# Kernel tuning notes

Hardware: AMD Instinct MI355X
Metric: run time of the kernel (lower is better)

The kernel has to match this reference:

```python
import jax, jax.numpy as jnp
import numpy as np

B, N, MW, H, C, K = 64, 8192, 128, 8, 1024, 3
HD = C // H  # head width = 128


def setup_inputs() -> dict:
    key = jax.random.key(0)
    ks = jax.random.split(key, 16)
    s = 0.02
    return {
        "control_state": jax.random.normal(ks[0], (B, C), jnp.float32),
        "memory": jax.random.normal(ks[1], (B, N, MW), jnp.float32),
        "prev_weights": jax.nn.softmax(jax.random.normal(ks[2], (B, H, N), jnp.float32), axis=-1),
        "defaults": jax.nn.softmax(jax.random.normal(ks[3], (B, H, N), jnp.float32), axis=-1),
        "W_head": s * jax.random.normal(ks[4], (C, H * HD), jnp.float32),
        "b_head": jnp.zeros((H, HD), jnp.float32),
        "W_reset": s * jax.random.normal(ks[5], (H, HD, 1), jnp.float32),
        "b_reset": jnp.zeros((H, 1), jnp.float32),
        "W_key": s * jax.random.normal(ks[6], (H, HD, MW), jnp.float32),
        "b_key": jnp.zeros((H, MW), jnp.float32),
        "W_beta": s * jax.random.normal(ks[7], (H, HD, 1), jnp.float32),
        "b_beta": jnp.zeros((H, 1), jnp.float32),
        "W_gate": s * jax.random.normal(ks[8], (H, HD, 1), jnp.float32),
        "b_gate": jnp.zeros((H, 1), jnp.float32),
        "W_shift": s * jax.random.normal(ks[9], (H, HD, K), jnp.float32),
        "b_shift": jnp.zeros((H, K), jnp.float32),
        "W_gamma": s * jax.random.normal(ks[10], (H, HD, 1), jnp.float32),
        "b_gamma": jnp.zeros((H, 1), jnp.float32),
        "merge_w": jax.random.normal(ks[11], (H,), jnp.float32) * 0.3 + 1.0 / H,
    }


def reference(control_state, memory, prev_weights, defaults, W_head, b_head,
              W_reset, b_reset, W_key, b_key, W_beta, b_beta, W_gate, b_gate,
              W_shift, b_shift, W_gamma, b_gamma, merge_w):
    eps = 1e-8
    # head projection: [B,C] -> [B,H,HD]
    heads = (control_state @ W_head).reshape(-1, H, HD) + b_head
    # sigmoid reset gate: convex blend of prior weights with defaults
    reset_p = jax.nn.sigmoid(jnp.einsum('bhd,hdo->bho', heads, W_reset) + b_reset)  # [B,H,1]
    weights = prev_weights * (1.0 - reset_p) + defaults * reset_p
    # NTM addressing parameters (per-head linear maps)
    key_ = jnp.einsum('bhd,hdw->bhw', heads, W_key) + b_key          # [B,H,MW]
    beta = jax.nn.softplus(jnp.einsum('bhd,hdo->bho', heads, W_beta) + b_beta)   # [B,H,1]
    gate = jax.nn.sigmoid(jnp.einsum('bhd,hdo->bho', heads, W_gate) + b_gate)    # [B,H,1]
    shift = jax.nn.softmax(jnp.einsum('bhd,hdk->bhk', heads, W_shift) + b_shift, axis=-1)  # [B,H,K]
    gamma = 1.0 + jax.nn.softplus(jnp.einsum('bhd,hdo->bho', heads, W_gamma) + b_gamma)    # [B,H,1]
    # content addressing: sharpened cosine similarity softmax over memory slots
    sim = jnp.einsum('bhw,bnw->bhn', key_, memory)
    sim = sim / (jnp.linalg.norm(key_, axis=-1, keepdims=True)
                 * jnp.linalg.norm(memory, axis=-1)[:, None, :] + eps)
    content = jax.nn.softmax(beta * sim, axis=-1)                    # [B,H,N]
    # interpolate with (possibly reset) prior weights
    w_g = gate * content + (1.0 - gate) * weights
    # location addressing: circular convolution with shift kernel symmetric around 0
    w_s = sum(shift[..., j:j + 1] * jnp.roll(w_g, j - K // 2, axis=-1) for j in range(K))
    # sharpening
    w_pow = (w_s + eps) ** gamma
    new_w = w_pow / jnp.sum(w_pow, axis=-1, keepdims=True)           # [B,H,N]
    # read: per-head attention matmul against memory, then weighted head merge
    headed = jnp.einsum('bhn,bnw->bhw', new_w, memory)               # [B,H,MW]
    out = jnp.einsum('bhw,h->bw', headed, merge_w)                   # [B,MW]
    return out, new_w
```

## Files before the change

### kernel.cpp

```cpp
#include <hip/hip_runtime.h>
#include <hip/hip_bf16.h>
#include <math.h>

#define Bb 64
#define Nn 8192
#define MWw 128
#define Hh 8
#define Cc 1024
#define HDd 128
#define Kk 3

__device__ __forceinline__ float dot4(float4 a, float4 b) {
  return a.x*b.x + a.y*b.y + a.z*b.z + a.w*b.w;
}
__device__ __forceinline__ float sigmoidf_(float x) { return 1.0f / (1.0f + __expf(-x)); }
__device__ __forceinline__ float softplusf_(float x) {
  return fmaxf(x, 0.0f) + log1pf(__expf(-fabsf(x)));
}

__global__ __launch_bounds__(1024) void k_params(
    const float* __restrict__ cs, const float* __restrict__ W_head, const float* __restrict__ b_head,
    const float* __restrict__ W_reset, const float* __restrict__ b_reset,
    const float* __restrict__ W_key, const float* __restrict__ b_key,
    const float* __restrict__ W_beta, const float* __restrict__ b_beta,
    const float* __restrict__ W_gate, const float* __restrict__ b_gate,
    const float* __restrict__ W_shift, const float* __restrict__ b_shift,
    const float* __restrict__ W_gamma, const float* __restrict__ b_gamma,
    float* __restrict__ key_ws, float* __restrict__ params)
{
  int bh = blockIdx.x;
  int b = bh >> 3, h = bh & 7;
  int t = threadIdx.x;
  int d = t & 127, sl = t >> 7;
  __shared__ float red[8][128];
  __shared__ float head_s[128];
  __shared__ float key_s[128];

  const float* csb = cs + b * Cc + sl * 128;
  const float* w0 = W_head + (size_t)(sl * 128) * (Hh * HDd) + h * HDd + d;
  float acc = 0.0f;
  #pragma unroll 8
  for (int c = 0; c < 128; ++c) acc = fmaf(csb[c], w0[(size_t)c * (Hh * HDd)], acc);
  red[sl][d] = acc;
  __syncthreads();
  if (t < 128) {
    float s = b_head[h * HDd + t];
    #pragma unroll
    for (int j = 0; j < 8; ++j) s += red[j][t];
    head_s[t] = s;
  }
  __syncthreads();

  {
    const float* wk = W_key + (size_t)h * HDd * MWw + (sl * 16) * MWw + d;
    float ka = 0.0f;
    #pragma unroll
    for (int dd = 0; dd < 16; ++dd) ka = fmaf(head_s[sl * 16 + dd], wk[dd * MWw], ka);
    red[sl][d] = ka;
  }
  __syncthreads();
  if (t < 128) {
    float kv = b_key[h * MWw + t];
    #pragma unroll
    for (int j = 0; j < 8; ++j) kv += red[j][t];
    key_ws[bh * MWw + t] = kv;
    key_s[t] = kv;
  }
  __syncthreads();

  float hd = head_s[d];
  float v;
  switch (sl) {
    case 0: v = hd * W_reset[h * HDd + d]; break;
    case 1: v = hd * W_beta[h * HDd + d]; break;
    case 2: v = hd * W_gate[h * HDd + d]; break;
    case 3: v = hd * W_gamma[h * HDd + d]; break;
    case 4: v = hd * W_shift[(h * HDd + d) * Kk + 0]; break;
    case 5: v = hd * W_shift[(h * HDd + d) * Kk + 1]; break;
    case 6: v = hd * W_shift[(h * HDd + d) * Kk + 2]; break;
    default: v = key_s[d] * key_s[d]; break;
  }
  red[sl][d] = v;
  __syncthreads();
  for (int s = 64; s > 0; s >>= 1) {
    if (d < s) red[sl][d] += red[sl][d + s];
    __syncthreads();
  }
  if (t == 0) {
    float reset = sigmoidf_(red[0][0] + b_reset[h]);
    float beta  = softplusf_(red[1][0] + b_beta[h]);
    float gate  = sigmoidf_(red[2][0] + b_gate[h]);
    float gamma = 1.0f + softplusf_(red[3][0] + b_gamma[h]);
    float a0 = red[4][0] + b_shift[h * Kk + 0];
    float a1 = red[5][0] + b_shift[h * Kk + 1];
    float a2 = red[6][0] + b_shift[h * Kk + 2];
    float mx = fmaxf(a0, fmaxf(a1, a2));
    float e0 = __expf(a0 - mx), e1 = __expf(a1 - mx), e2 = __expf(a2 - mx);
    float inv = 1.0f / (e0 + e1 + e2);
    float* P = params + bh * 8;
    P[0] = reset; P[1] = beta; P[2] = gate; P[3] = gamma;
    P[4] = e0 * inv; P[5] = e1 * inv; P[6] = e2 * inv;
    P[7] = sqrtf(red[7][0]);
  }
}

__global__ __launch_bounds__(256, 2) void k_sim(
    const float* __restrict__ mem, const float* __restrict__ key_ws,
    const float* __restrict__ params, float* __restrict__ e_ws, float* __restrict__ Z)
{
  int b = blockIdx.y, chunk = blockIdx.x;
  int t = threadIdx.x;
  int lane = t & 63, wid = t >> 6;
  int sub = lane & 7, rid = lane >> 3;
  __shared__ float4 keys[8][32];
  __shared__ float betas[8], knorms[8];
  if (t < 8) { betas[t] = params[(b * 8 + t) * 8 + 1]; knorms[t] = params[(b * 8 + t) * 8 + 7]; }
  {
    int h = t >> 5, q = t & 31;
    keys[h][q] = ((const float4*)key_ws)[(b * 8 + h) * 32 + q];
  }
  __syncthreads();

  float4 kreg[8][4];
  #pragma unroll
  for (int h2 = 0; h2 < 8; ++h2) {
    kreg[h2][0] = keys[h2][sub];
    kreg[h2][1] = keys[h2][sub + 8];
    kreg[h2][2] = keys[h2][sub + 16];
    kreg[h2][3] = keys[h2][sub + 24];
  }

  const float4* m4 = (const float4*)mem + (size_t)b * Nn * 32;
  float beta = betas[sub], kn = knorms[sub];
  float zloc = 0.0f;
  int n0 = chunk * 512;

  #pragma unroll 1
  for (int itr = 0; itr < 8; ++itr) {
    int nb = n0 + itr * 64 + wid * 16 + rid;
    float4 m[2][4];
    float nrm[2];
    float acc[2][8];
    #pragma unroll
    for (int r = 0; r < 2; ++r) {
      const float4* rp = m4 + (size_t)(nb + r * 8) * 32 + sub;
      m[r][0] = rp[0]; m[r][1] = rp[8]; m[r][2] = rp[16]; m[r][3] = rp[24];
    }
    #pragma unroll
    for (int r = 0; r < 2; ++r) {
      nrm[r] = dot4(m[r][0], m[r][0]) + dot4(m[r][1], m[r][1])
             + dot4(m[r][2], m[r][2]) + dot4(m[r][3], m[r][3]);
      #pragma unroll
      for (int h2 = 0; h2 < 8; ++h2) {
        acc[r][h2] = dot4(m[r][0], kreg[h2][0]) + dot4(m[r][1], kreg[h2][1])
                   + dot4(m[r][2], kreg[h2][2]) + dot4(m[r][3], kreg[h2][3]);
      }
    }
    #pragma unroll
    for (int r = 0; r < 2; ++r) {
      float* a = acc[r];
      bool h1 = (sub & 1) != 0;
      float v40 = (h1 ? a[1] : a[0]) + __shfl_xor(h1 ? a[0] : a[1], 1, 64);
      float v41 = (h1 ? a[3] : a[2]) + __shfl_xor(h1 ? a[2] : a[3], 1, 64);
      float v42 = (h1 ? a[5] : a[4]) + __shfl_xor(h1 ? a[4] : a[5], 1, 64);
      float v43 = (h1 ? a[7] : a[6]) + __shfl_xor(h1 ? a[6] : a[7], 1, 64);
      bool h2b = (sub & 2) != 0;
      float v20 = (h2b ? v41 : v40) + __shfl_xor(h2b ? v40 : v41, 2, 64);
      float v21 = (h2b ? v43 : v42) + __shfl_xor(h2b ? v42 : v43, 2, 64);
      bool h4 = (sub & 4) != 0;
      float dsum = (h4 ? v21 : v20) + __shfl_xor(h4 ? v20 : v21, 4, 64);
      float nr = nrm[r];
      nr += __shfl_xor(nr, 1, 64);
      nr += __shfl_xor(nr, 2, 64);
      nr += __shfl_xor(nr, 4, 64);
      float s = beta * dsum / (kn * sqrtf(nr) + 1e-8f);
      float e = __expf(s - beta);
      e_ws[(size_t)(b * 8 + sub) * Nn + (nb + r * 8)] = e;
      zloc += e;
    }
  }
  zloc += __shfl_xor(zloc, 8, 64);
  zloc += __shfl_xor(zloc, 16, 64);
  zloc += __shfl_xor(zloc, 32, 64);
  if (lane < 8) atomicAdd(&Z[b * 8 + lane], zloc);
}

__global__ __launch_bounds__(256) void k_conv(
    const float* __restrict__ e_ws, const float* __restrict__ prev, const float* __restrict__ defw,
    const float* __restrict__ params, const float* __restrict__ Z,
    float* __restrict__ wp, float* __restrict__ S)
{
  int chunk = blockIdx.x, h = blockIdx.y, b = blockIdx.z;
  int bh = b * 8 + h, t = threadIdx.x;
  __shared__ float wg[2050];
  const float* P = params + bh * 8;
  float reset = P[0], gate = P[2], gamma = P[3], s0 = P[4], s1 = P[5], s2 = P[6];
  float invZg = gate / Z[bh];
  float om = 1.0f - gate, omr = 1.0f - reset;
  size_t base = (size_t)bh * Nn;
  int n0 = chunk * 2048;

  for (int it = 0; it < 8; ++it) {
    int l = it * 256 + t;
    int n = n0 + l;
    float e = e_ws[base + n], pv = prev[base + n], dv = defw[base + n];
    wg[1 + l] = invZg * e + om * (pv * omr + dv * reset);
  }
  if (t < 2) {
    int n = (t == 0) ? ((n0 + Nn - 1) & (Nn - 1)) : ((n0 + 2048) & (Nn - 1));
    float e = e_ws[base + n], pv = prev[base + n], dv = defw[base + n];
    wg[(t == 0) ? 0 : 2049] = invZg * e + om * (pv * omr + dv * reset);
  }
  __syncthreads();

  float sacc = 0.0f;
  for (int it = 0; it < 8; ++it) {
    int l = it * 256 + t;
    float wsv = s0 * wg[l + 2] + s1 * wg[l + 1] + s2 * wg[l];
    float wpv = __expf(gamma * __logf(wsv + 1e-8f));
    wp[base + n0 + l] = wpv;
    sacc += wpv;
  }
  sacc += __shfl_xor(sacc, 1, 64);
  sacc += __shfl_xor(sacc, 2, 64);
  sacc += __shfl_xor(sacc, 4, 64);
  sacc += __shfl_xor(sacc, 8, 64);
  sacc += __shfl_xor(sacc, 16, 64);
  sacc += __shfl_xor(sacc, 32, 64);
  __shared__ float sred[4];
  if ((t & 63) == 0) sred[t >> 6] = sacc;
  __syncthreads();
  if (t == 0) atomicAdd(&S[bh], sred[0] + sred[1] + sred[2] + sred[3]);
}

__global__ __launch_bounds__(256) void k_norm(
    float* __restrict__ wp, const float* __restrict__ S, const float* __restrict__ merge_w,
    float* __restrict__ coef)
{
  int b = blockIdx.y; int n0 = blockIdx.x * 1024; int t = threadIdx.x;
  __shared__ float invS[8], mw[8];
  if (t < 8) { invS[t] = 1.0f / S[b * 8 + t]; mw[t] = merge_w[t]; }
  __syncthreads();
  for (int it = 0; it < 4; ++it) {
    int n = n0 + it * 256 + t;
    float cf = 0.0f;
    #pragma unroll
    for (int h = 0; h < 8; ++h) {
      size_t idx = (size_t)(b * 8 + h) * Nn + n;
      float v = wp[idx] * invS[h];
      wp[idx] = v;
      cf = fmaf(mw[h], v, cf);
    }
    coef[(size_t)b * Nn + n] = cf;
  }
}

__global__ __launch_bounds__(256) void k_read(
    const float* __restrict__ mem, const float* __restrict__ coef, float* __restrict__ out)
{
  int b = blockIdx.y; int n0 = blockIdx.x * 512; int t = threadIdx.x;
  int w4 = t & 31, rg = t >> 5;
  const float4* m4 = (const float4*)mem + (size_t)b * Nn * 32;
  const float* cf = coef + (size_t)b * Nn;
  float4 acc = make_float4(0.0f, 0.0f, 0.0f, 0.0f);
  #pragma unroll 4
  for (int it = 0; it < 64; ++it) {
    int n = n0 + it * 8 + rg;
    float c = cf[n];
    float4 m = m4[(size_t)n * 32 + w4];
    acc.x = fmaf(c, m.x, acc.x);
    acc.y = fmaf(c, m.y, acc.y);
    acc.z = fmaf(c, m.z, acc.z);
    acc.w = fmaf(c, m.w, acc.w);
  }
  __shared__ float4 red4[256];
  red4[t] = acc;
  __syncthreads();
  if (t < 32) {
    float4 s = red4[t];
    #pragma unroll
    for (int j = 1; j < 8; ++j) {
      float4 o = red4[t + 32 * j];
      s.x += o.x; s.y += o.y; s.z += o.z; s.w += o.w;
    }
    atomicAdd(&out[b * MWw + t * 4 + 0], s.x);
    atomicAdd(&out[b * MWw + t * 4 + 1], s.y);
    atomicAdd(&out[b * MWw + t * 4 + 2], s.z);
    atomicAdd(&out[b * MWw + t * 4 + 3], s.w);
  }
}

extern "C" void kernel_launch(void* const* d_in, const int* in_sizes, int n_in,
                              void* d_out, int out_size, void* d_ws, size_t ws_size,
                              hipStream_t stream)
{
  const float* cs      = (const float*)d_in[0];
  const float* mem     = (const float*)d_in[1];
  const float* prev    = (const float*)d_in[2];
  const float* defw    = (const float*)d_in[3];
  const float* W_head  = (const float*)d_in[4];
  const float* b_head  = (const float*)d_in[5];
  const float* W_reset = (const float*)d_in[6];
  const float* b_reset = (const float*)d_in[7];
  const float* W_key   = (const float*)d_in[8];
  const float* b_key   = (const float*)d_in[9];
  const float* W_beta  = (const float*)d_in[10];
  const float* b_beta  = (const float*)d_in[11];
  const float* W_gate  = (const float*)d_in[12];
  const float* b_gate  = (const float*)d_in[13];
  const float* W_shift = (const float*)d_in[14];
  const float* b_shift = (const float*)d_in[15];
  const float* W_gamma = (const float*)d_in[16];
  const float* b_gamma = (const float*)d_in[17];
  const float* merge_w = (const float*)d_in[18];

  float* out  = (float*)d_out;
  float* neww = out + Bb * MWw;

  float* ws_f   = (float*)d_ws;
  float* key_ws = ws_f;
  float* params = ws_f + 65536;
  float* Zacc   = ws_f + 69632;
  float* Sacc   = ws_f + 70144;
  float* e_ws   = ws_f + 70656;
  float* coef   = ws_f + 70656 + 4194304;

  hipMemsetAsync(Zacc, 0, 1024 * sizeof(float), stream);
  hipMemsetAsync(out, 0, Bb * MWw * sizeof(float), stream);

  k_params<<<dim3(Bb * Hh), dim3(1024), 0, stream>>>(
      cs, W_head, b_head, W_reset, b_reset, W_key, b_key, W_beta, b_beta,
      W_gate, b_gate, W_shift, b_shift, W_gamma, b_gamma, key_ws, params);
  k_sim<<<dim3(16, Bb), dim3(256), 0, stream>>>(mem, key_ws, params, e_ws, Zacc);
  k_conv<<<dim3(4, Hh, Bb), dim3(256), 0, stream>>>(e_ws, prev, defw, params, Zacc, neww, Sacc);
  k_norm<<<dim3(8, Bb), dim3(256), 0, stream>>>(neww, Sacc, merge_w, coef);
  k_read<<<dim3(16, Bb), dim3(256), 0, stream>>>(mem, coef, out);
}
```

Before: 505.6 us.

## Fuse normalization into read kernel, stage sim outputs in LDS, vectorize conv

Merges the weight-normalization kernel into the memory-read kernel, so the per-slot coefficient lives in shared memory instead of a global workspace buffer and one launch is dropped. The similarity kernel now buffers its exp values in shared memory and writes them out as coalesced float4 rows instead of strided scalar stores. The convolution/sharpen kernel is rewritten to use float4 loads and stores, with the halo elements kept at the end of the shared buffer. In exchange, the similarity kernel uses more shared memory, which may lower occupancy.

```diff
diff --git a/kernel.cpp b/kernel.cpp
--- a/kernel.cpp
+++ b/kernel.cpp
@@ -114,6 +114,7 @@
   int sub = lane & 7, rid = lane >> 3;
   __shared__ float4 keys[8][32];
   __shared__ float betas[8], knorms[8];
+  __shared__ float e_s[8][520];
   if (t < 8) { betas[t] = params[(b * 8 + t) * 8 + 1]; knorms[t] = params[(b * 8 + t) * 8 + 7]; }
   {
     int h = t >> 5, q = t & 31;
@@ -175,7 +176,7 @@
       nr += __shfl_xor(nr, 4, 64);
       float s = beta * dsum / (kn * sqrtf(nr) + 1e-8f);
       float e = __expf(s - beta);
-      e_ws[(size_t)(b * 8 + sub) * Nn + (nb + r * 8)] = e;
+      e_s[sub][(nb + r * 8) - n0] = e;
       zloc += e;
     }
   }
@@ -183,6 +184,15 @@
   zloc += __shfl_xor(zloc, 16, 64);
   zloc += __shfl_xor(zloc, 32, 64);
   if (lane < 8) atomicAdd(&Z[b * 8 + lane], zloc);
+  __syncthreads();
+
+  #pragma unroll
+  for (int j = 0; j < 4; ++j) {
+    int idx = j * 256 + t;
+    int h = idx >> 7, q = idx & 127;
+    float4 v = *(const float4*)&e_s[h][q * 4];
+    ((float4*)(e_ws + (size_t)(b * 8 + h) * Nn + n0))[q] = v;
+  }
 }
 
 __global__ __launch_bounds__(256) void k_conv(
@@ -192,7 +202,7 @@
 {
   int chunk = blockIdx.x, h = blockIdx.y, b = blockIdx.z;
   int bh = b * 8 + h, t = threadIdx.x;
-  __shared__ float wg[2050];
+  __shared__ float wg[2052];
   const float* P = params + bh * 8;
   float reset = P[0], gate = P[2], gamma = P[3], s0 = P[4], s1 = P[5], s2 = P[6];
   float invZg = gate / Z[bh];
@@ -200,26 +210,48 @@
   size_t base = (size_t)bh * Nn;
   int n0 = chunk * 2048;
 
-  for (int it = 0; it < 8; ++it) {
-    int l = it * 256 + t;
-    int n = n0 + l;
-    float e = e_ws[base + n], pv = prev[base + n], dv = defw[base + n];
-    wg[1 + l] = invZg * e + om * (pv * omr + dv * reset);
+  const float4* e4p = (const float4*)(e_ws + base + n0);
+  const float4* p4p = (const float4*)(prev + base + n0);
+  const float4* d4p = (const float4*)(defw + base + n0);
+  #pragma unroll
+  for (int it = 0; it < 2; ++it) {
+    int idx4 = it * 256 + t;
+    float4 e = e4p[idx4], pv = p4p[idx4], dv = d4p[idx4];
+    float4 w;
+    w.x = invZg * e.x + om * (pv.x * omr + dv.x * reset);
+    w.y = invZg * e.y + om * (pv.y * omr + dv.y * reset);
+    w.z = invZg * e.z + om * (pv.z * omr + dv.z * reset);
+    w.w = invZg * e.w + om * (pv.w * omr + dv.w * reset);
+    *(float4*)&wg[idx4 * 4] = w;
   }
   if (t < 2) {
     int n = (t == 0) ? ((n0 + Nn - 1) & (Nn - 1)) : ((n0 + 2048) & (Nn - 1));
     float e = e_ws[base + n], pv = prev[base + n], dv = defw[base + n];
-    wg[(t == 0) ? 0 : 2049] = invZg * e + om * (pv * omr + dv * reset);
+    wg[2048 + t] = invZg * e + om * (pv * omr + dv * reset);
   }
   __syncthreads();
 
   float sacc = 0.0f;
-  for (int it = 0; it < 8; ++it) {
-    int l = it * 256 + t;
-    float wsv = s0 * wg[l + 2] + s1 * wg[l + 1] + s2 * wg[l];
-    float wpv = __expf(gamma * __logf(wsv + 1e-8f));
-    wp[base + n0 + l] = wpv;
-    sacc += wpv;
+  float4* wp4 = (float4*)(wp + base + n0);
+  #pragma unroll
+  for (int it = 0; it < 2; ++it) {
+    int idx4 = it * 256 + t;
+    int l = idx4 * 4;
+    float4 c = *(const float4*)&wg[l];
+    float left  = (l == 0)        ? wg[2048] : wg[l - 1];
+    float right = (l + 4 == 2048) ? wg[2049] : wg[l + 4];
+    float4 wsv;
+    wsv.x = s0 * c.y   + s1 * c.x + s2 * left;
+    wsv.y = s0 * c.z   + s1 * c.y + s2 * c.x;
+    wsv.z = s0 * c.w   + s1 * c.z + s2 * c.y;
+    wsv.w = s0 * right + s1 * c.w + s2 * c.z;
+    float4 o;
+    o.x = __expf(gamma * __logf(wsv.x + 1e-8f));
+    o.y = __expf(gamma * __logf(wsv.y + 1e-8f));
+    o.z = __expf(gamma * __logf(wsv.z + 1e-8f));
+    o.w = __expf(gamma * __logf(wsv.w + 1e-8f));
+    wp4[idx4] = o;
+    sacc += o.x + o.y + o.z + o.w;
   }
   sacc += __shfl_xor(sacc, 1, 64);
   sacc += __shfl_xor(sacc, 2, 64);
@@ -233,47 +265,49 @@
   if (t == 0) atomicAdd(&S[bh], sred[0] + sred[1] + sred[2] + sred[3]);
 }
 
-__global__ __launch_bounds__(256) void k_norm(
-    float* __restrict__ wp, const float* __restrict__ S, const float* __restrict__ merge_w,
-    float* __restrict__ coef)
-{
-  int b = blockIdx.y; int n0 = blockIdx.x * 1024; int t = threadIdx.x;
-  __shared__ float invS[8], mw[8];
-  if (t < 8) { invS[t] = 1.0f / S[b * 8 + t]; mw[t] = merge_w[t]; }
-  __syncthreads();
-  for (int it = 0; it < 4; ++it) {
-    int n = n0 + it * 256 + t;
+__global__ __launch_bounds__(256) void k_readnorm(
+    const float* __restrict__ mem, float* __restrict__ wp, const float* __restrict__ S,
+    const float* __restrict__ merge_w, float* __restrict__ out)
+{
+  int b = blockIdx.y; int n0 = blockIdx.x * 512; int t = threadIdx.x;
+  __shared__ float kh[8], invS_s[8];
+  __shared__ float coef_s[512];
+  __shared__ float4 red4[256];
+  if (t < 8) {
+    float s = S[b * 8 + t];
+    invS_s[t] = 1.0f / s;
+    kh[t] = merge_w[t] / s;
+  }
+  __syncthreads();
+
+  #pragma unroll
+  for (int ii = 0; ii < 2; ++ii) {
+    int nl = ii * 256 + t;
     float cf = 0.0f;
     #pragma unroll
     for (int h = 0; h < 8; ++h) {
-      size_t idx = (size_t)(b * 8 + h) * Nn + n;
-      float v = wp[idx] * invS[h];
-      wp[idx] = v;
-      cf = fmaf(mw[h], v, cf);
-    }
-    coef[(size_t)b * Nn + n] = cf;
-  }
-}
-
-__global__ __launch_bounds__(256) void k_read(
-    const float* __restrict__ mem, const float* __restrict__ coef, float* __restrict__ out)
-{
-  int b = blockIdx.y; int n0 = blockIdx.x * 512; int t = threadIdx.x;
+      size_t idx = (size_t)(b * 8 + h) * Nn + n0 + nl;
+      float v = wp[idx];
+      wp[idx] = v * invS_s[h];
+      cf = fmaf(kh[h], v, cf);
+    }
+    coef_s[nl] = cf;
+  }
+  __syncthreads();
+
   int w4 = t & 31, rg = t >> 5;
   const float4* m4 = (const float4*)mem + (size_t)b * Nn * 32;
-  const float* cf = coef + (size_t)b * Nn;
   float4 acc = make_float4(0.0f, 0.0f, 0.0f, 0.0f);
   #pragma unroll 4
   for (int it = 0; it < 64; ++it) {
-    int n = n0 + it * 8 + rg;
-    float c = cf[n];
-    float4 m = m4[(size_t)n * 32 + w4];
+    int nl = it * 8 + rg;
+    float c = coef_s[nl];
+    float4 m = m4[(size_t)(n0 + nl) * 32 + w4];
     acc.x = fmaf(c, m.x, acc.x);
     acc.y = fmaf(c, m.y, acc.y);
     acc.z = fmaf(c, m.z, acc.z);
     acc.w = fmaf(c, m.w, acc.w);
   }
-  __shared__ float4 red4[256];
   red4[t] = acc;
   __syncthreads();
   if (t < 32) {
@@ -323,7 +357,6 @@
   float* Zacc   = ws_f + 69632;
   float* Sacc   = ws_f + 70144;
   float* e_ws   = ws_f + 70656;
-  float* coef   = ws_f + 70656 + 4194304;
 
   hipMemsetAsync(Zacc, 0, 1024 * sizeof(float), stream);
   hipMemsetAsync(out, 0, Bb * MWw * sizeof(float), stream);
@@ -333,6 +366,5 @@
       W_gate, b_gate, W_shift, b_shift, W_gamma, b_gamma, key_ws, params);
   k_sim<<<dim3(16, Bb), dim3(256), 0, stream>>>(mem, key_ws, params, e_ws, Zacc);
   k_conv<<<dim3(4, Hh, Bb), dim3(256), 0, stream>>>(e_ws, prev, defw, params, Zacc, neww, Sacc);
-  k_norm<<<dim3(8, Bb), dim3(256), 0, stream>>>(neww, Sacc, merge_w, coef);
-  k_read<<<dim3(16, Bb), dim3(256), 0, stream>>>(mem, coef, out);
-}
+  k_readnorm<<<dim3(16, Bb), dim3(256), 0, stream>>>(mem, neww, Sacc, merge_w, out);
+}
```

After: 502.6 us. Within noise of the previous version (-0.6%).
